# Optimization experiments

Measured on AMD Instinct MI355X. Metric: run time of the kernel, lower is better.

## Reference

```python
import jax, jax.numpy as jnp
import numpy as np

N_NODES = 50000
N_EDGES = 800000
D = 128


def setup_inputs() -> dict:
    key = jax.random.key(0)
    ks = jax.random.split(key, 7)
    return {
        "shape_features": jax.random.normal(ks[0], (N_NODES, D), dtype=jnp.float32),
        "W1": jax.random.normal(ks[1], (D, D), dtype=jnp.float32) * 0.05,
        "b1": jax.random.normal(ks[2], (D,), dtype=jnp.float32) * 0.05,
        "W2": jax.random.normal(ks[3], (D, D), dtype=jnp.float32) * 0.05,
        "b2": jax.random.normal(ks[4], (D,), dtype=jnp.float32) * 0.05,
        "edge_src": jax.random.randint(ks[5], (N_EDGES,), 0, N_NODES, dtype=jnp.int32),
        "edge_dst": jax.random.randint(ks[6], (N_EDGES,), 0, N_NODES, dtype=jnp.int32),
    }


def reference(shape_features, W1, b1, W2, b2, edge_src, edge_dst):
    # out1 = linear1(x)  (torch Linear: x @ W.T + b)
    out1 = jnp.einsum("nd,od->no", shape_features, W1) + b1
    # ragged neighbour gather + sum per destination node (segment reduce)
    aggr = jax.ops.segment_sum(shape_features[edge_src], edge_dst,
                               num_segments=shape_features.shape[0])
    # out = linear1(x) + linear2(aggr)
    return out1 + jnp.einsum("nd,od->no", aggr, W2) + b2
```

## Files before the change

### kernel.cpp

```cpp
#include <hip/hip_runtime.h>
#include <hip/hip_bf16.h>

#define DF 128
#define BSH 5
#define BNODES 32
#define NBMAX 2048
#define CHUNK 8192
#define BMAX 128
#define TILE 2048
#define ASTRIDE 68
#define SRCMASK 0x07ffffffu

typedef __attribute__((ext_vector_type(8))) short short8;
typedef __attribute__((ext_vector_type(4))) float floatx4;

__device__ __forceinline__ ushort f2bf(float f) {
    __hip_bfloat16 h = __float2bfloat16(f);
    return *reinterpret_cast<ushort*>(&h);
}

__global__ __launch_bounds__(256) void prep_kernel(
    const float* __restrict__ x, ushort* __restrict__ xbf, int n4,
    const float* __restrict__ W1, const float* __restrict__ W2,
    const float* __restrict__ b1, const float* __restrict__ b2,
    ushort* __restrict__ w1bf, ushort* __restrict__ w2bf, float* __restrict__ bias,
    const int* __restrict__ dst, int* __restrict__ histG,
    int n_edges, int B_, int nb)
{
    __shared__ int h[NBMAX];
    int bid = blockIdx.x;
    if (bid < B_) {
        for (int j = threadIdx.x; j < nb; j += 256) h[j] = 0;
        __syncthreads();
        int base = bid * CHUNK;
#pragma unroll 4
        for (int i = 0; i < CHUNK / 256; ++i) {
            int e = base + i * 256 + threadIdx.x;
            if (e < n_edges) atomicAdd(&h[dst[e] >> BSH], 1);
        }
        __syncthreads();
        for (int j = threadIdx.x; j < nb; j += 256)
            histG[bid * nb + j] = h[j];
    } else if (bid < B_ + 64) {
        int i = (bid - B_) * 256 + threadIdx.x;
        if (i < DF * DF) {
            w1bf[i] = f2bf(W1[i]);
            w2bf[i] = f2bf(W2[i]);
        }
        if (i < DF) bias[i] = b1[i] + b2[i];
    } else {
        int i = (bid - B_ - 64) * 256 + threadIdx.x;
        if (i < n4) {
            float4 v = reinterpret_cast<const float4*>(x)[i];
            ushort4 o;
            o.x = f2bf(v.x); o.y = f2bf(v.y); o.z = f2bf(v.z); o.w = f2bf(v.w);
            reinterpret_cast<ushort4*>(xbf)[i] = o;
        }
    }
}

__global__ __launch_bounds__(256) void scan_local_kernel(
    const int* __restrict__ cnt, int* __restrict__ offs,
    int* __restrict__ bsum, int n)
{
    __shared__ int sd[256];
    int t = threadIdx.x;
    int base = blockIdx.x * 1024 + t * 4;

    int4 v = make_int4(0, 0, 0, 0);
    if (base + 3 < n) {
        v = *reinterpret_cast<const int4*>(cnt + base);
    } else {
        if (base + 0 < n) v.x = cnt[base + 0];
        if (base + 1 < n) v.y = cnt[base + 1];
        if (base + 2 < n) v.z = cnt[base + 2];
        if (base + 3 < n) v.w = cnt[base + 3];
    }
    int s = v.x + v.y + v.z + v.w;
    sd[t] = s;
    __syncthreads();
    for (int off = 1; off < 256; off <<= 1) {
        int u = (t >= off) ? sd[t - off] : 0;
        __syncthreads();
        sd[t] += u;
        __syncthreads();
    }
    int incl = sd[t];
    int excl = incl - s;
    if (t == 255) bsum[blockIdx.x] = incl;

    int p0 = excl, p1 = p0 + v.x, p2 = p1 + v.y, p3 = p2 + v.z;
    if (base + 0 < n) offs[base + 0] = p0;
    if (base + 1 < n) offs[base + 1] = p1;
    if (base + 2 < n) offs[base + 2] = p2;
    if (base + 3 < n) offs[base + 3] = p3;
}

__global__ __launch_bounds__(1024) void scan_bsum_kernel(
    int* __restrict__ bsum, int nb2)
{
    __shared__ int sd[1024];
    int t = threadIdx.x;
    int v = (t < nb2) ? bsum[t] : 0;
    sd[t] = v;
    __syncthreads();
    for (int off = 1; off < 1024; off <<= 1) {
        int u = (t >= off) ? sd[t - off] : 0;
        __syncthreads();
        sd[t] += u;
        __syncthreads();
    }
    if (t < nb2) bsum[t] = sd[t] - v;
}

__global__ __launch_bounds__(1024) void bin_kernel(
    const int* __restrict__ src, const int* __restrict__ dst,
    const int* __restrict__ histS, const int* __restrict__ bsum,
    uint* __restrict__ pairs, int n_edges, int B_, int nb)
{
    __shared__ int  cur[NBMAX];
    __shared__ uint stage[CHUNK];
    int blk = blockIdx.x;
    for (int j = threadIdx.x; j < nb; j += 1024) {
        int idx = blk * nb + j;
        cur[j] = histS[idx] + bsum[idx >> 10];
    }
    __syncthreads();
    int base = blk * CHUNK;
    int cnt = n_edges - base; if (cnt > CHUNK) cnt = CHUNK;
    for (int i = threadIdx.x; i < cnt; i += 1024) {
        int e = base + i;
        int d = dst[e];
        int j = d >> BSH;
        int p = atomicAdd(&cur[j], 1);
        stage[p - base] = (uint)src[e] | ((uint)(d & (BNODES - 1)) << 27);
    }
    __syncthreads();
    for (int i = threadIdx.x; i < cnt; i += 1024)
        pairs[base + i] = stage[i];
}

__global__ __launch_bounds__(256) void agg_gemm_kernel(
    const ushort* __restrict__ xbf, const uint* __restrict__ pairs,
    const int* __restrict__ histS, const int* __restrict__ bsum,
    const ushort* __restrict__ w1, const ushort* __restrict__ w2,
    const float* __restrict__ bias, float* __restrict__ out,
    int n_nodes, int n_edges, int B_, int nb, int flat)
{
    __shared__ uint raw[TILE];
    __shared__ uint sorted[TILE];
    __shared__ uint abuf[BNODES * ASTRIDE];
    __shared__ int  rstart[BMAX];
    __shared__ int  rexcl[BMAX + 1];
    __shared__ int hcnt[BNODES];
    __shared__ int hoff[BNODES + 1];
    __shared__ int hcur[BNODES];

    int blk  = blockIdx.x;
    int node0 = blk * BNODES;
    int wave = threadIdx.x >> 6;
    int lane = threadIdx.x & 63;

    auto loadOffs = [&](int idx) -> int {
        if (idx >= flat) return n_edges;
        return histS[idx] + bsum[idx >> 10];
    };

    if (threadIdx.x < B_) {
        int idx = threadIdx.x * nb + blk;
        int s = loadOffs(idx);
        rstart[threadIdx.x] = s;
        rexcl[threadIdx.x]  = loadOffs(idx + 1) - s;
    }
    __syncthreads();
    if (threadIdx.x < 64) {
        int c0 = (lane < B_) ? rexcl[lane] : 0;
        int c1 = (64 + lane < B_) ? rexcl[64 + lane] : 0;
        int s0 = c0, s1 = c1;
#pragma unroll
        for (int off = 1; off < 64; off <<= 1) {
            int u0 = __shfl_up(s0, off);
            int u1 = __shfl_up(s1, off);
            if (lane >= off) { s0 += u0; s1 += u1; }
        }
        int t0 = __shfl(s0, 63);
        int t1 = __shfl(s1, 63);
        if (lane < B_) rexcl[lane] = s0 - c0;
        if (64 + lane < B_) rexcl[64 + lane] = t0 + s1 - c1;
        if (lane == 0) rexcl[B_] = t0 + t1;
    }
    __syncthreads();
    int total = rexcl[B_];

    const uint* xv = reinterpret_cast<const uint*>(xbf);
    float2 acc[8];
#pragma unroll
    for (int i = 0; i < 8; ++i) acc[i] = make_float2(0.f, 0.f);

    for (int t0 = 0; t0 < total; t0 += TILE) {
        int cnt = total - t0; if (cnt > TILE) cnt = TILE;

        if (threadIdx.x < BNODES) hcnt[threadIdx.x] = 0;
        __syncthreads();

        for (int i = threadIdx.x; i < cnt; i += 256) {
            int t = t0 + i;
            int lo = 0, hi = B_;
            while (lo + 1 < hi) {
                int mid = (lo + hi) >> 1;
                if (rexcl[mid] <= t) lo = mid; else hi = mid;
            }
            uint pk = pairs[rstart[lo] + (t - rexcl[lo])];
            raw[i] = pk;
            atomicAdd(&hcnt[pk >> 27], 1);
        }
        __syncthreads();

        if (threadIdx.x < 64) {
            int v = (lane < BNODES) ? hcnt[lane] : 0;
#pragma unroll
            for (int off = 1; off < BNODES; off <<= 1) {
                int u = __shfl_up(v, off);
                if (lane >= off) v += u;
            }
            if (lane < BNODES) {
                hoff[lane + 1] = v;
                hcur[lane] = v - hcnt[lane];
            }
            if (lane == 0) hoff[0] = 0;
        }
        __syncthreads();

        for (int i = threadIdx.x; i < cnt; i += 256) {
            uint pk = raw[i];
            int p = atomicAdd(&hcur[pk >> 27], 1);
            sorted[p] = pk & SRCMASK;
        }
        __syncthreads();

#pragma unroll
        for (int i = 0; i < 8; ++i) {
            int nl = wave * 8 + i;
            int j0 = hoff[nl], j1 = hoff[nl + 1];
            float2 a = acc[i];
            int j = j0;
            for (; j + 7 < j1; j += 8) {
                uint u0 = xv[(size_t)sorted[j + 0] * 64 + lane];
                uint u1 = xv[(size_t)sorted[j + 1] * 64 + lane];
                uint u2 = xv[(size_t)sorted[j + 2] * 64 + lane];
                uint u3 = xv[(size_t)sorted[j + 3] * 64 + lane];
                uint u4 = xv[(size_t)sorted[j + 4] * 64 + lane];
                uint u5 = xv[(size_t)sorted[j + 5] * 64 + lane];
                uint u6 = xv[(size_t)sorted[j + 6] * 64 + lane];
                uint u7 = xv[(size_t)sorted[j + 7] * 64 + lane];
                a.x += __uint_as_float(u0 << 16) + __uint_as_float(u1 << 16)
                     + __uint_as_float(u2 << 16) + __uint_as_float(u3 << 16)
                     + __uint_as_float(u4 << 16) + __uint_as_float(u5 << 16)
                     + __uint_as_float(u6 << 16) + __uint_as_float(u7 << 16);
                a.y += __uint_as_float(u0 & 0xffff0000u) + __uint_as_float(u1 & 0xffff0000u)
                     + __uint_as_float(u2 & 0xffff0000u) + __uint_as_float(u3 & 0xffff0000u)
                     + __uint_as_float(u4 & 0xffff0000u) + __uint_as_float(u5 & 0xffff0000u)
                     + __uint_as_float(u6 & 0xffff0000u) + __uint_as_float(u7 & 0xffff0000u);
            }
            for (; j + 3 < j1; j += 4) {
                uint u0 = xv[(size_t)sorted[j + 0] * 64 + lane];
                uint u1 = xv[(size_t)sorted[j + 1] * 64 + lane];
                uint u2 = xv[(size_t)sorted[j + 2] * 64 + lane];
                uint u3 = xv[(size_t)sorted[j + 3] * 64 + lane];
                a.x += __uint_as_float(u0 << 16) + __uint_as_float(u1 << 16)
                     + __uint_as_float(u2 << 16) + __uint_as_float(u3 << 16);
                a.y += __uint_as_float(u0 & 0xffff0000u) + __uint_as_float(u1 & 0xffff0000u)
                     + __uint_as_float(u2 & 0xffff0000u) + __uint_as_float(u3 & 0xffff0000u);
            }
            for (; j < j1; ++j) {
                uint u = xv[(size_t)sorted[j] * 64 + lane];
                a.x += __uint_as_float(u << 16);
                a.y += __uint_as_float(u & 0xffff0000u);
            }
            acc[i] = a;
        }
        __syncthreads();
    }

#pragma unroll
    for (int i = 0; i < 8; ++i) {
        int nl = wave * 8 + i;
        abuf[nl * ASTRIDE + lane] =
            (uint)f2bf(acc[i].x) | ((uint)f2bf(acc[i].y) << 16);
    }
    __syncthreads();

    int quad = lane >> 4;
    int m    = lane & 15;
    int rg   = wave >> 1;
    int half = wave & 1;
    int rowL = rg * 16 + m;
    int rowG = node0 + rowL;
    int rowC = (rowG < n_nodes) ? rowG : (n_nodes - 1);

    short8 xa[4], aa[4];
#pragma unroll
    for (int ks = 0; ks < 4; ++ks) {
        xa[ks] = *reinterpret_cast<const short8*>(xbf + (size_t)rowC * DF + ks * 32 + quad * 8);
        aa[ks] = *reinterpret_cast<const short8*>(&abuf[rowL * ASTRIDE + ks * 16 + quad * 4]);
    }

    int nbase = node0 + rg * 16;
#pragma unroll
    for (int oi = 0; oi < 4; ++oi) {
        int ot = half * 4 + oi;
        int o = ot * 16 + m;
        floatx4 c = {0.f, 0.f, 0.f, 0.f};
#pragma unroll
        for (int ks = 0; ks < 4; ++ks) {
            short8 bf1 = *reinterpret_cast<const short8*>(w1 + (size_t)o * DF + ks * 32 + quad * 8);
            short8 bf2 = *reinterpret_cast<const short8*>(w2 + (size_t)o * DF + ks * 32 + quad * 8);
            c = __builtin_amdgcn_mfma_f32_16x16x32_bf16(xa[ks], bf1, c, 0, 0, 0);
            c = __builtin_amdgcn_mfma_f32_16x16x32_bf16(aa[ks], bf2, c, 0, 0, 0);
        }
        float bv = bias[o];
#pragma unroll
        for (int r = 0; r < 4; ++r) {
            int row = nbase + quad * 4 + r;
            if (row < n_nodes) out[(size_t)row * DF + o] = c[r] + bv;
        }
    }
}

extern "C" void kernel_launch(void* const* d_in, const int* in_sizes, int n_in,
                              void* d_out, int out_size, void* d_ws, size_t ws_size,
                              hipStream_t stream) {
    const float* x  = (const float*)d_in[0];
    const float* W1 = (const float*)d_in[1];
    const float* b1 = (const float*)d_in[2];
    const float* W2 = (const float*)d_in[3];
    const float* b2 = (const float*)d_in[4];
    const int* esrc = (const int*)d_in[5];
    const int* edst = (const int*)d_in[6];
    float* out = (float*)d_out;

    int n_nodes = in_sizes[0] / DF;
    int n_edges = in_sizes[5];

    int nb = (n_nodes + BNODES - 1) >> BSH;
    int B_ = (n_edges + CHUNK - 1) / CHUNK;
    int flat = nb * B_;

    char* ws = (char*)d_ws;
    ushort* xbf   = (ushort*)ws;                 ws += (size_t)n_nodes * DF * 2;
    ushort* w1bf  = (ushort*)ws;                 ws += (size_t)DF * DF * 2;
    ushort* w2bf  = (ushort*)ws;                 ws += (size_t)DF * DF * 2;
    float*  bias  = (float*)ws;                  ws += (size_t)DF * 4;
    int*    histG = (int*)ws;                    ws += (size_t)flat * 4;
    int*    histS = (int*)ws;                    ws += (size_t)(flat + 1) * 4;
    int*    bsum  = (int*)ws;                    ws += 1024 * 4;
    uint*   pairs = (uint*)ws;

    int n4 = n_nodes * DF / 4;
    int prep_blocks = B_ + 64 + (n4 + 255) / 256;
    prep_kernel<<<prep_blocks, 256, 0, stream>>>(
        x, xbf, n4, W1, W2, b1, b2, w1bf, w2bf, bias,
        edst, histG, n_edges, B_, nb);

    int nb2 = (flat + 1023) / 1024;
    scan_local_kernel<<<nb2, 256, 0, stream>>>(histG, histS, bsum, flat);
    scan_bsum_kernel<<<1, 1024, 0, stream>>>(bsum, nb2);

    bin_kernel<<<B_, 1024, 0, stream>>>(esrc, edst, histS, bsum, pairs, n_edges, B_, nb);

    agg_gemm_kernel<<<nb, 256, 0, stream>>>(
        xbf, pairs, histS, bsum, w1bf, w2bf, bias, out,
        n_nodes, n_edges, B_, nb, flat);
}
```

Before: 178.0 us.

## Replace per-chunk histogram scans with global atomic histogram and last-block scan

```diff
diff --git a/kernel.cpp b/kernel.cpp
--- a/kernel.cpp
+++ b/kernel.cpp
@@ -5,8 +5,8 @@
 #define BSH 5
 #define BNODES 32
 #define NBMAX 2048
-#define CHUNK 8192
-#define BMAX 128
+#define PCHUNK 8192
+#define BCHUNK 4096
 #define TILE 2048
 #define ASTRIDE 68
 #define SRCMASK 0x07ffffffu
@@ -24,32 +24,69 @@
     const float* __restrict__ W1, const float* __restrict__ W2,
     const float* __restrict__ b1, const float* __restrict__ b2,
     ushort* __restrict__ w1bf, ushort* __restrict__ w2bf, float* __restrict__ bias,
-    const int* __restrict__ dst, int* __restrict__ histG,
-    int n_edges, int B_, int nb)
+    const int* __restrict__ dst, int* __restrict__ ghist, int* __restrict__ done,
+    int* __restrict__ gbase, int* __restrict__ gcur,
+    int n_edges, int PH, int nb)
 {
     __shared__ int h[NBMAX];
+    __shared__ int isLast;
     int bid = blockIdx.x;
-    if (bid < B_) {
+    if (bid < PH) {
         for (int j = threadIdx.x; j < nb; j += 256) h[j] = 0;
         __syncthreads();
-        int base = bid * CHUNK;
+        int base = bid * PCHUNK;
 #pragma unroll 4
-        for (int i = 0; i < CHUNK / 256; ++i) {
+        for (int i = 0; i < PCHUNK / 256; ++i) {
             int e = base + i * 256 + threadIdx.x;
             if (e < n_edges) atomicAdd(&h[dst[e] >> BSH], 1);
         }
         __syncthreads();
-        for (int j = threadIdx.x; j < nb; j += 256)
-            histG[bid * nb + j] = h[j];
-    } else if (bid < B_ + 64) {
-        int i = (bid - B_) * 256 + threadIdx.x;
+        for (int j = threadIdx.x; j < nb; j += 256) {
+            int c = h[j];
+            if (c) atomicAdd(&ghist[j], c);
+        }
+        __threadfence();
+        __syncthreads();
+        if (threadIdx.x == 0) isLast = (atomicAdd(done, 1) == PH - 1);
+        __syncthreads();
+        if (isLast) {
+            int b0 = threadIdx.x * 8;
+            int vals[8];
+            int s = 0;
+#pragma unroll
+            for (int k = 0; k < 8; ++k) {
+                int idx = b0 + k;
+                int v = (idx < nb)
+                    ? __hip_atomic_load(&ghist[idx], __ATOMIC_RELAXED,
+                                        __HIP_MEMORY_SCOPE_AGENT)
+                    : 0;
+                vals[k] = v; s += v;
+            }
+            h[threadIdx.x] = s;
+            __syncthreads();
+            for (int off = 1; off < 256; off <<= 1) {
+                int u = (threadIdx.x >= off) ? h[threadIdx.x - off] : 0;
+                __syncthreads();
+                h[threadIdx.x] += u;
+                __syncthreads();
+            }
+            int run = h[threadIdx.x] - s;
+#pragma unroll
+            for (int k = 0; k < 8; ++k) {
+                int idx = b0 + k;
+                if (idx < nb) { gbase[idx] = run; gcur[idx] = run; run += vals[k]; }
+            }
+            if (threadIdx.x == 0) gbase[nb] = n_edges;
+        }
+    } else if (bid < PH + 64) {
+        int i = (bid - PH) * 256 + threadIdx.x;
         if (i < DF * DF) {
             w1bf[i] = f2bf(W1[i]);
             w2bf[i] = f2bf(W2[i]);
         }
         if (i < DF) bias[i] = b1[i] + b2[i];
     } else {
-        int i = (bid - B_ - 64) * 256 + threadIdx.x;
+        int i = (bid - PH - 64) * 256 + threadIdx.x;
         if (i < n4) {
             float4 v = reinterpret_cast<const float4*>(x)[i];
             ushort4 o;
@@ -59,160 +96,81 @@
     }
 }
 
-__global__ __launch_bounds__(256) void scan_local_kernel(
-    const int* __restrict__ cnt, int* __restrict__ offs,
-    int* __restrict__ bsum, int n)
+__global__ __launch_bounds__(512) void bin_kernel(
+    const int* __restrict__ src, const int* __restrict__ dst,
+    int* __restrict__ gcur, uint* __restrict__ pairs, int n_edges, int nb)
 {
-    __shared__ int sd[256];
-    int t = threadIdx.x;
-    int base = blockIdx.x * 1024 + t * 4;
-
-    int4 v = make_int4(0, 0, 0, 0);
-    if (base + 3 < n) {
-        v = *reinterpret_cast<const int4*>(cnt + base);
-    } else {
-        if (base + 0 < n) v.x = cnt[base + 0];
-        if (base + 1 < n) v.y = cnt[base + 1];
-        if (base + 2 < n) v.z = cnt[base + 2];
-        if (base + 3 < n) v.w = cnt[base + 3];
-    }
-    int s = v.x + v.y + v.z + v.w;
-    sd[t] = s;
+    __shared__ int h[NBMAX];
+    int tid = threadIdx.x;
+    for (int j = tid; j < nb; j += 512) h[j] = 0;
     __syncthreads();
-    for (int off = 1; off < 256; off <<= 1) {
-        int u = (t >= off) ? sd[t - off] : 0;
-        __syncthreads();
-        sd[t] += u;
-        __syncthreads();
-    }
-    int incl = sd[t];
-    int excl = incl - s;
-    if (t == 255) bsum[blockIdx.x] = incl;
-
-    int p0 = excl, p1 = p0 + v.x, p2 = p1 + v.y, p3 = p2 + v.z;
-    if (base + 0 < n) offs[base + 0] = p0;
-    if (base + 1 < n) offs[base + 1] = p1;
-    if (base + 2 < n) offs[base + 2] = p2;
-    if (base + 3 < n) offs[base + 3] = p3;
-}
-
-__global__ __launch_bounds__(1024) void scan_bsum_kernel(
-    int* __restrict__ bsum, int nb2)
+    int base = blockIdx.x * BCHUNK;
+    int d[8], sv[8];
+#pragma unroll
+    for (int k = 0; k < 8; ++k) {
+        int i = base + k * 512 + tid;
+        bool ok = i < n_edges;
+        d[k]  = ok ? dst[i] : -1;
+        sv[k] = ok ? src[i] : 0;
+        if (ok) atomicAdd(&h[d[k] >> BSH], 1);
+    }
+    __syncthreads();
+    for (int j = tid; j < nb; j += 512) {
+        int c = h[j];
+        if (c) h[j] = atomicAdd(&gcur[j], c);
+    }
+    __syncthreads();
+#pragma unroll
+    for (int k = 0; k < 8; ++k) {
+        if (d[k] >= 0) {
+            int p = atomicAdd(&h[d[k] >> BSH], 1);
+            pairs[p] = (uint)sv[k] | ((uint)(d[k] & (BNODES - 1)) << 27);
+        }
+    }
+}
+
+__global__ __launch_bounds__(256, 6) void agg_gemm_kernel(
+    const ushort* __restrict__ xbf, const uint* __restrict__ pairs,
+    const int* __restrict__ gbase,
+    const ushort* __restrict__ w1, const ushort* __restrict__ w2,
+    const float* __restrict__ bias, float* __restrict__ out, int n_nodes)
 {
-    __shared__ int sd[1024];
-    int t = threadIdx.x;
-    int v = (t < nb2) ? bsum[t] : 0;
-    sd[t] = v;
-    __syncthreads();
-    for (int off = 1; off < 1024; off <<= 1) {
-        int u = (t >= off) ? sd[t - off] : 0;
-        __syncthreads();
-        sd[t] += u;
-        __syncthreads();
-    }
-    if (t < nb2) bsum[t] = sd[t] - v;
-}
-
-__global__ __launch_bounds__(1024) void bin_kernel(
-    const int* __restrict__ src, const int* __restrict__ dst,
-    const int* __restrict__ histS, const int* __restrict__ bsum,
-    uint* __restrict__ pairs, int n_edges, int B_, int nb)
-{
-    __shared__ int  cur[NBMAX];
-    __shared__ uint stage[CHUNK];
-    int blk = blockIdx.x;
-    for (int j = threadIdx.x; j < nb; j += 1024) {
-        int idx = blk * nb + j;
-        cur[j] = histS[idx] + bsum[idx >> 10];
-    }
-    __syncthreads();
-    int base = blk * CHUNK;
-    int cnt = n_edges - base; if (cnt > CHUNK) cnt = CHUNK;
-    for (int i = threadIdx.x; i < cnt; i += 1024) {
-        int e = base + i;
-        int d = dst[e];
-        int j = d >> BSH;
-        int p = atomicAdd(&cur[j], 1);
-        stage[p - base] = (uint)src[e] | ((uint)(d & (BNODES - 1)) << 27);
-    }
-    __syncthreads();
-    for (int i = threadIdx.x; i < cnt; i += 1024)
-        pairs[base + i] = stage[i];
-}
-
-__global__ __launch_bounds__(256) void agg_gemm_kernel(
-    const ushort* __restrict__ xbf, const uint* __restrict__ pairs,
-    const int* __restrict__ histS, const int* __restrict__ bsum,
-    const ushort* __restrict__ w1, const ushort* __restrict__ w2,
-    const float* __restrict__ bias, float* __restrict__ out,
-    int n_nodes, int n_edges, int B_, int nb, int flat)
-{
-    __shared__ uint raw[TILE];
     __shared__ uint sorted[TILE];
     __shared__ uint abuf[BNODES * ASTRIDE];
-    __shared__ int  rstart[BMAX];
-    __shared__ int  rexcl[BMAX + 1];
     __shared__ int hcnt[BNODES];
     __shared__ int hoff[BNODES + 1];
     __shared__ int hcur[BNODES];
 
-    int blk  = blockIdx.x;
+    int blk   = blockIdx.x;
     int node0 = blk * BNODES;
-    int wave = threadIdx.x >> 6;
-    int lane = threadIdx.x & 63;
-
-    auto loadOffs = [&](int idx) -> int {
-        if (idx >= flat) return n_edges;
-        return histS[idx] + bsum[idx >> 10];
-    };
-
-    if (threadIdx.x < B_) {
-        int idx = threadIdx.x * nb + blk;
-        int s = loadOffs(idx);
-        rstart[threadIdx.x] = s;
-        rexcl[threadIdx.x]  = loadOffs(idx + 1) - s;
-    }
-    __syncthreads();
-    if (threadIdx.x < 64) {
-        int c0 = (lane < B_) ? rexcl[lane] : 0;
-        int c1 = (64 + lane < B_) ? rexcl[64 + lane] : 0;
-        int s0 = c0, s1 = c1;
-#pragma unroll
-        for (int off = 1; off < 64; off <<= 1) {
-            int u0 = __shfl_up(s0, off);
-            int u1 = __shfl_up(s1, off);
-            if (lane >= off) { s0 += u0; s1 += u1; }
-        }
-        int t0 = __shfl(s0, 63);
-        int t1 = __shfl(s1, 63);
-        if (lane < B_) rexcl[lane] = s0 - c0;
-        if (64 + lane < B_) rexcl[64 + lane] = t0 + s1 - c1;
-        if (lane == 0) rexcl[B_] = t0 + t1;
-    }
-    __syncthreads();
-    int total = rexcl[B_];
-
-    const uint* xv = reinterpret_cast<const uint*>(xbf);
+    int wave  = threadIdx.x >> 6;
+    int lane  = threadIdx.x & 63;
+
+    int start = gbase[blk];
+    int end   = gbase[blk + 1];
+
+    const char* xu = (const char*)xbf;
+    uint lane4 = (uint)lane << 2;
+
     float2 acc[8];
 #pragma unroll
     for (int i = 0; i < 8; ++i) acc[i] = make_float2(0.f, 0.f);
 
-    for (int t0 = 0; t0 < total; t0 += TILE) {
-        int cnt = total - t0; if (cnt > TILE) cnt = TILE;
+    for (int t0 = start; t0 < end; t0 += TILE) {
+        int cnt = end - t0; if (cnt > TILE) cnt = TILE;
 
         if (threadIdx.x < BNODES) hcnt[threadIdx.x] = 0;
         __syncthreads();
 
-        for (int i = threadIdx.x; i < cnt; i += 256) {
-            int t = t0 + i;
-            int lo = 0, hi = B_;
-            while (lo + 1 < hi) {
-                int mid = (lo + hi) >> 1;
-                if (rexcl[mid] <= t) lo = mid; else hi = mid;
-            }
-            uint pk = pairs[rstart[lo] + (t - rexcl[lo])];
-            raw[i] = pk;
-            atomicAdd(&hcnt[pk >> 27], 1);
+        uint pk_[8];
+#pragma unroll
+        for (int k = 0; k < 8; ++k) {
+            int i = threadIdx.x + k * 256;
+            if (i < cnt) {
+                uint pk = pairs[t0 + i];
+                pk_[k] = pk;
+                atomicAdd(&hcnt[pk >> 27], 1);
+            }
         }
         __syncthreads();
 
@@ -231,10 +189,14 @@
         }
         __syncthreads();
 
-        for (int i = threadIdx.x; i < cnt; i += 256) {
-            uint pk = raw[i];
-            int p = atomicAdd(&hcur[pk >> 27], 1);
-            sorted[p] = pk & SRCMASK;
+#pragma unroll
+        for (int k = 0; k < 8; ++k) {
+            int i = threadIdx.x + k * 256;
+            if (i < cnt) {
+                uint pk = pk_[k];
+                int p = atomicAdd(&hcur[pk >> 27], 1);
+                sorted[p] = (pk & SRCMASK) << 8;
+            }
         }
         __syncthreads();
 
@@ -244,36 +206,29 @@
             int j0 = hoff[nl], j1 = hoff[nl + 1];
             float2 a = acc[i];
             int j = j0;
-            for (; j + 7 < j1; j += 8) {
-                uint u0 = xv[(size_t)sorted[j + 0] * 64 + lane];
-                uint u1 = xv[(size_t)sorted[j + 1] * 64 + lane];
-                uint u2 = xv[(size_t)sorted[j + 2] * 64 + lane];
-                uint u3 = xv[(size_t)sorted[j + 3] * 64 + lane];
-                uint u4 = xv[(size_t)sorted[j + 4] * 64 + lane];
-                uint u5 = xv[(size_t)sorted[j + 5] * 64 + lane];
-                uint u6 = xv[(size_t)sorted[j + 6] * 64 + lane];
-                uint u7 = xv[(size_t)sorted[j + 7] * 64 + lane];
-                a.x += __uint_as_float(u0 << 16) + __uint_as_float(u1 << 16)
-                     + __uint_as_float(u2 << 16) + __uint_as_float(u3 << 16)
-                     + __uint_as_float(u4 << 16) + __uint_as_float(u5 << 16)
-                     + __uint_as_float(u6 << 16) + __uint_as_float(u7 << 16);
-                a.y += __uint_as_float(u0 & 0xffff0000u) + __uint_as_float(u1 & 0xffff0000u)
-                     + __uint_as_float(u2 & 0xffff0000u) + __uint_as_float(u3 & 0xffff0000u)
-                     + __uint_as_float(u4 & 0xffff0000u) + __uint_as_float(u5 & 0xffff0000u)
-                     + __uint_as_float(u6 & 0xffff0000u) + __uint_as_float(u7 & 0xffff0000u);
+            for (; j + 15 < j1; j += 16) {
+                uint u[16];
+#pragma unroll
+                for (int k = 0; k < 16; ++k)
+                    u[k] = *(const uint*)(xu + (size_t)(sorted[j + k] + lane4));
+#pragma unroll
+                for (int k = 0; k < 16; ++k) {
+                    a.x += __uint_as_float(u[k] << 16);
+                    a.y += __uint_as_float(u[k] & 0xffff0000u);
+                }
             }
             for (; j + 3 < j1; j += 4) {
-                uint u0 = xv[(size_t)sorted[j + 0] * 64 + lane];
-                uint u1 = xv[(size_t)sorted[j + 1] * 64 + lane];
-                uint u2 = xv[(size_t)sorted[j + 2] * 64 + lane];
-                uint u3 = xv[(size_t)sorted[j + 3] * 64 + lane];
+                uint u0 = *(const uint*)(xu + (size_t)(sorted[j + 0] + lane4));
+                uint u1 = *(const uint*)(xu + (size_t)(sorted[j + 1] + lane4));
+                uint u2 = *(const uint*)(xu + (size_t)(sorted[j + 2] + lane4));
+                uint u3 = *(const uint*)(xu + (size_t)(sorted[j + 3] + lane4));
                 a.x += __uint_as_float(u0 << 16) + __uint_as_float(u1 << 16)
                      + __uint_as_float(u2 << 16) + __uint_as_float(u3 << 16);
                 a.y += __uint_as_float(u0 & 0xffff0000u) + __uint_as_float(u1 & 0xffff0000u)
                      + __uint_as_float(u2 & 0xffff0000u) + __uint_as_float(u3 & 0xffff0000u);
             }
             for (; j < j1; ++j) {
-                uint u = xv[(size_t)sorted[j] * 64 + lane];
+                uint u = *(const uint*)(xu + (size_t)(sorted[j] + lane4));
                 a.x += __uint_as_float(u << 16);
                 a.y += __uint_as_float(u & 0xffff0000u);
             }
@@ -343,32 +298,30 @@
     int n_edges = in_sizes[5];
 
     int nb = (n_nodes + BNODES - 1) >> BSH;
-    int B_ = (n_edges + CHUNK - 1) / CHUNK;
-    int flat = nb * B_;
+    int PH = (n_edges + PCHUNK - 1) / PCHUNK;
+    int BB = (n_edges + BCHUNK - 1) / BCHUNK;
 
     char* ws = (char*)d_ws;
     ushort* xbf   = (ushort*)ws;                 ws += (size_t)n_nodes * DF * 2;
     ushort* w1bf  = (ushort*)ws;                 ws += (size_t)DF * DF * 2;
     ushort* w2bf  = (ushort*)ws;                 ws += (size_t)DF * DF * 2;
     float*  bias  = (float*)ws;                  ws += (size_t)DF * 4;
-    int*    histG = (int*)ws;                    ws += (size_t)flat * 4;
-    int*    histS = (int*)ws;                    ws += (size_t)(flat + 1) * 4;
-    int*    bsum  = (int*)ws;                    ws += 1024 * 4;
+    int*    ghist = (int*)ws;                    ws += (size_t)(nb + 1) * 4;
+    int*    done  = ghist + nb;
+    int*    gbase = (int*)ws;                    ws += (size_t)(nb + 1) * 4;
+    int*    gcur  = (int*)ws;                    ws += (size_t)nb * 4;
     uint*   pairs = (uint*)ws;
 
+    hipMemsetAsync(ghist, 0, (size_t)(nb + 1) * sizeof(int), stream);
+
     int n4 = n_nodes * DF / 4;
-    int prep_blocks = B_ + 64 + (n4 + 255) / 256;
+    int prep_blocks = PH + 64 + (n4 + 255) / 256;
     prep_kernel<<<prep_blocks, 256, 0, stream>>>(
         x, xbf, n4, W1, W2, b1, b2, w1bf, w2bf, bias,
-        edst, histG, n_edges, B_, nb);
-
-    int nb2 = (flat + 1023) / 1024;
-    scan_local_kernel<<<nb2, 256, 0, stream>>>(histG, histS, bsum, flat);
-    scan_bsum_kernel<<<1, 1024, 0, stream>>>(bsum, nb2);
-
-    bin_kernel<<<B_, 1024, 0, stream>>>(esrc, edst, histS, bsum, pairs, n_edges, B_, nb);
+        edst, ghist, done, gbase, gcur, n_edges, PH, nb);
+
+    bin_kernel<<<BB, 512, 0, stream>>>(esrc, edst, gcur, pairs, n_edges, nb);
 
     agg_gemm_kernel<<<nb, 256, 0, stream>>>(
-        xbf, pairs, histS, bsum, w1bf, w2bf, bias, out,
-        n_nodes, n_edges, B_, nb, flat);
-}
+        xbf, pairs, gbase, w1bf, w2bf, bias, out, n_nodes);
+}
```

Result: slower. 188.1 us (+5.7%).

## Shrink node blocks to 16, fuse scan kernels, and widen gather unroll

Applied to the files above, without the earlier changes.

```diff
diff --git a/kernel.cpp b/kernel.cpp
--- a/kernel.cpp
+++ b/kernel.cpp
@@ -2,12 +2,12 @@
 #include <hip/hip_bf16.h>
 
 #define DF 128
-#define BSH 5
-#define BNODES 32
-#define NBMAX 2048
+#define BSH 4
+#define BNODES 16
+#define NBMAX 4096
 #define CHUNK 8192
 #define BMAX 128
-#define TILE 2048
+#define TILE 1024
 #define ASTRIDE 68
 #define SRCMASK 0x07ffffffu
 
@@ -24,7 +24,7 @@
     const float* __restrict__ W1, const float* __restrict__ W2,
     const float* __restrict__ b1, const float* __restrict__ b2,
     ushort* __restrict__ w1bf, ushort* __restrict__ w2bf, float* __restrict__ bias,
-    const int* __restrict__ dst, int* __restrict__ histG,
+    const int* __restrict__ dst, int* __restrict__ histG, int* __restrict__ sdone,
     int n_edges, int B_, int nb)
 {
     __shared__ int h[NBMAX];
@@ -48,6 +48,7 @@
             w2bf[i] = f2bf(W2[i]);
         }
         if (i < DF) bias[i] = b1[i] + b2[i];
+        if (bid == B_ && threadIdx.x == 0) *sdone = 0;
     } else {
         int i = (bid - B_ - 64) * 256 + threadIdx.x;
         if (i < n4) {
@@ -59,11 +60,12 @@
     }
 }
 
-__global__ __launch_bounds__(256) void scan_local_kernel(
+__global__ __launch_bounds__(256) void scan_kernel(
     const int* __restrict__ cnt, int* __restrict__ offs,
-    int* __restrict__ bsum, int n)
+    int* __restrict__ bsum, int* __restrict__ sdone, int n, int nb2)
 {
     __shared__ int sd[256];
+    __shared__ int isLast;
     int t = threadIdx.x;
     int base = blockIdx.x * 1024 + t * 4;
 
@@ -94,23 +96,40 @@
     if (base + 1 < n) offs[base + 1] = p1;
     if (base + 2 < n) offs[base + 2] = p2;
     if (base + 3 < n) offs[base + 3] = p3;
-}
-
-__global__ __launch_bounds__(1024) void scan_bsum_kernel(
-    int* __restrict__ bsum, int nb2)
-{
-    __shared__ int sd[1024];
-    int t = threadIdx.x;
-    int v = (t < nb2) ? bsum[t] : 0;
-    sd[t] = v;
-    __syncthreads();
-    for (int off = 1; off < 1024; off <<= 1) {
-        int u = (t >= off) ? sd[t - off] : 0;
-        __syncthreads();
-        sd[t] += u;
-        __syncthreads();
-    }
-    if (t < nb2) bsum[t] = sd[t] - v;
+
+    __threadfence();
+    __syncthreads();
+    if (t == 0) isLast = (atomicAdd(sdone, 1) == gridDim.x - 1);
+    __syncthreads();
+    if (isLast && t < 64) {
+        int b0 = t * 8;
+        int tv[8];
+        int run = 0;
+#pragma unroll
+        for (int k = 0; k < 8; ++k) {
+            int idx = b0 + k;
+            int u = (idx < nb2)
+                ? __hip_atomic_load(&bsum[idx], __ATOMIC_RELAXED,
+                                    __HIP_MEMORY_SCOPE_AGENT)
+                : 0;
+            tv[k] = u; run += u;
+        }
+        int laneTot = run;
+        int sI = laneTot;
+#pragma unroll
+        for (int off = 1; off < 64; off <<= 1) {
+            int u = __shfl_up(sI, off);
+            if (t >= off) sI += u;
+        }
+        int laneExcl = sI - laneTot;
+        int acc = laneExcl;
+#pragma unroll
+        for (int k = 0; k < 8; ++k) {
+            int idx = b0 + k;
+            if (idx < nb2) bsum[idx] = acc;
+            acc += tv[k];
+        }
+    }
 }
 
 __global__ __launch_bounds__(1024) void bin_kernel(
@@ -140,14 +159,13 @@
         pairs[base + i] = stage[i];
 }
 
-__global__ __launch_bounds__(256) void agg_gemm_kernel(
+__global__ __launch_bounds__(256, 6) void agg_gemm_kernel(
     const ushort* __restrict__ xbf, const uint* __restrict__ pairs,
     const int* __restrict__ histS, const int* __restrict__ bsum,
     const ushort* __restrict__ w1, const ushort* __restrict__ w2,
     const float* __restrict__ bias, float* __restrict__ out,
     int n_nodes, int n_edges, int B_, int nb, int flat)
 {
-    __shared__ uint raw[TILE];
     __shared__ uint sorted[TILE];
     __shared__ uint abuf[BNODES * ASTRIDE];
     __shared__ int  rstart[BMAX];
@@ -192,10 +210,12 @@
     __syncthreads();
     int total = rexcl[B_];
 
-    const uint* xv = reinterpret_cast<const uint*>(xbf);
-    float2 acc[8];
-#pragma unroll
-    for (int i = 0; i < 8; ++i) acc[i] = make_float2(0.f, 0.f);
+    const char* xu = (const char*)xbf;
+    uint lane4 = (uint)lane << 2;
+
+    float2 acc[4];
+#pragma unroll
+    for (int i = 0; i < 4; ++i) acc[i] = make_float2(0.f, 0.f);
 
     for (int t0 = 0; t0 < total; t0 += TILE) {
         int cnt = total - t0; if (cnt > TILE) cnt = TILE;
@@ -203,16 +223,21 @@
         if (threadIdx.x < BNODES) hcnt[threadIdx.x] = 0;
         __syncthreads();
 
-        for (int i = threadIdx.x; i < cnt; i += 256) {
-            int t = t0 + i;
-            int lo = 0, hi = B_;
-            while (lo + 1 < hi) {
-                int mid = (lo + hi) >> 1;
-                if (rexcl[mid] <= t) lo = mid; else hi = mid;
-            }
-            uint pk = pairs[rstart[lo] + (t - rexcl[lo])];
-            raw[i] = pk;
-            atomicAdd(&hcnt[pk >> 27], 1);
+        uint pk_[TILE / 256];
+#pragma unroll
+        for (int k = 0; k < TILE / 256; ++k) {
+            int i = threadIdx.x + k * 256;
+            if (i < cnt) {
+                int t = t0 + i;
+                int lo = 0, hi = B_;
+                while (lo + 1 < hi) {
+                    int mid = (lo + hi) >> 1;
+                    if (rexcl[mid] <= t) lo = mid; else hi = mid;
+                }
+                uint pk = pairs[rstart[lo] + (t - rexcl[lo])];
+                pk_[k] = pk;
+                atomicAdd(&hcnt[pk >> 27], 1);
+            }
         }
         __syncthreads();
 
@@ -231,49 +256,46 @@
         }
         __syncthreads();
 
-        for (int i = threadIdx.x; i < cnt; i += 256) {
-            uint pk = raw[i];
-            int p = atomicAdd(&hcur[pk >> 27], 1);
-            sorted[p] = pk & SRCMASK;
-        }
-        __syncthreads();
-
-#pragma unroll
-        for (int i = 0; i < 8; ++i) {
-            int nl = wave * 8 + i;
+#pragma unroll
+        for (int k = 0; k < TILE / 256; ++k) {
+            int i = threadIdx.x + k * 256;
+            if (i < cnt) {
+                uint pk = pk_[k];
+                int p = atomicAdd(&hcur[pk >> 27], 1);
+                sorted[p] = (pk & SRCMASK) << 8;
+            }
+        }
+        __syncthreads();
+
+#pragma unroll
+        for (int i = 0; i < 4; ++i) {
+            int nl = wave * 4 + i;
             int j0 = hoff[nl], j1 = hoff[nl + 1];
             float2 a = acc[i];
             int j = j0;
-            for (; j + 7 < j1; j += 8) {
-                uint u0 = xv[(size_t)sorted[j + 0] * 64 + lane];
-                uint u1 = xv[(size_t)sorted[j + 1] * 64 + lane];
-                uint u2 = xv[(size_t)sorted[j + 2] * 64 + lane];
-                uint u3 = xv[(size_t)sorted[j + 3] * 64 + lane];
-                uint u4 = xv[(size_t)sorted[j + 4] * 64 + lane];
-                uint u5 = xv[(size_t)sorted[j + 5] * 64 + lane];
-                uint u6 = xv[(size_t)sorted[j + 6] * 64 + lane];
-                uint u7 = xv[(size_t)sorted[j + 7] * 64 + lane];
-                a.x += __uint_as_float(u0 << 16) + __uint_as_float(u1 << 16)
-                     + __uint_as_float(u2 << 16) + __uint_as_float(u3 << 16)
-                     + __uint_as_float(u4 << 16) + __uint_as_float(u5 << 16)
-                     + __uint_as_float(u6 << 16) + __uint_as_float(u7 << 16);
-                a.y += __uint_as_float(u0 & 0xffff0000u) + __uint_as_float(u1 & 0xffff0000u)
-                     + __uint_as_float(u2 & 0xffff0000u) + __uint_as_float(u3 & 0xffff0000u)
-                     + __uint_as_float(u4 & 0xffff0000u) + __uint_as_float(u5 & 0xffff0000u)
-                     + __uint_as_float(u6 & 0xffff0000u) + __uint_as_float(u7 & 0xffff0000u);
+            for (; j + 15 < j1; j += 16) {
+                uint u[16];
+#pragma unroll
+                for (int k = 0; k < 16; ++k)
+                    u[k] = *(const uint*)(xu + (size_t)(sorted[j + k] + lane4));
+#pragma unroll
+                for (int k = 0; k < 16; ++k) {
+                    a.x += __uint_as_float(u[k] << 16);
+                    a.y += __uint_as_float(u[k] & 0xffff0000u);
+                }
             }
             for (; j + 3 < j1; j += 4) {
-                uint u0 = xv[(size_t)sorted[j + 0] * 64 + lane];
-                uint u1 = xv[(size_t)sorted[j + 1] * 64 + lane];
-                uint u2 = xv[(size_t)sorted[j + 2] * 64 + lane];
-                uint u3 = xv[(size_t)sorted[j + 3] * 64 + lane];
+                uint u0 = *(const uint*)(xu + (size_t)(sorted[j + 0] + lane4));
+                uint u1 = *(const uint*)(xu + (size_t)(sorted[j + 1] + lane4));
+                uint u2 = *(const uint*)(xu + (size_t)(sorted[j + 2] + lane4));
+                uint u3 = *(const uint*)(xu + (size_t)(sorted[j + 3] + lane4));
                 a.x += __uint_as_float(u0 << 16) + __uint_as_float(u1 << 16)
                      + __uint_as_float(u2 << 16) + __uint_as_float(u3 << 16);
                 a.y += __uint_as_float(u0 & 0xffff0000u) + __uint_as_float(u1 & 0xffff0000u)
                      + __uint_as_float(u2 & 0xffff0000u) + __uint_as_float(u3 & 0xffff0000u);
             }
             for (; j < j1; ++j) {
-                uint u = xv[(size_t)sorted[j] * 64 + lane];
+                uint u = *(const uint*)(xu + (size_t)(sorted[j] + lane4));
                 a.x += __uint_as_float(u << 16);
                 a.y += __uint_as_float(u & 0xffff0000u);
             }
@@ -283,8 +305,8 @@
     }
 
 #pragma unroll
-    for (int i = 0; i < 8; ++i) {
-        int nl = wave * 8 + i;
+    for (int i = 0; i < 4; ++i) {
+        int nl = wave * 4 + i;
         abuf[nl * ASTRIDE + lane] =
             (uint)f2bf(acc[i].x) | ((uint)f2bf(acc[i].y) << 16);
     }
@@ -292,23 +314,19 @@
 
     int quad = lane >> 4;
     int m    = lane & 15;
-    int rg   = wave >> 1;
-    int half = wave & 1;
-    int rowL = rg * 16 + m;
-    int rowG = node0 + rowL;
+    int rowG = node0 + m;
     int rowC = (rowG < n_nodes) ? rowG : (n_nodes - 1);
 
     short8 xa[4], aa[4];
 #pragma unroll
     for (int ks = 0; ks < 4; ++ks) {
         xa[ks] = *reinterpret_cast<const short8*>(xbf + (size_t)rowC * DF + ks * 32 + quad * 8);
-        aa[ks] = *reinterpret_cast<const short8*>(&abuf[rowL * ASTRIDE + ks * 16 + quad * 4]);
-    }
-
-    int nbase = node0 + rg * 16;
-#pragma unroll
-    for (int oi = 0; oi < 4; ++oi) {
-        int ot = half * 4 + oi;
+        aa[ks] = *reinterpret_cast<const short8*>(&abuf[m * ASTRIDE + ks * 16 + quad * 4]);
+    }
+
+#pragma unroll
+    for (int oi = 0; oi < 2; ++oi) {
+        int ot = wave * 2 + oi;
         int o = ot * 16 + m;
         floatx4 c = {0.f, 0.f, 0.f, 0.f};
 #pragma unroll
@@ -321,7 +339,7 @@
         float bv = bias[o];
 #pragma unroll
         for (int r = 0; r < 4; ++r) {
-            int row = nbase + quad * 4 + r;
+            int row = node0 + quad * 4 + r;
             if (row < n_nodes) out[(size_t)row * DF + o] = c[r] + bv;
         }
     }
@@ -353,18 +371,18 @@
     float*  bias  = (float*)ws;                  ws += (size_t)DF * 4;
     int*    histG = (int*)ws;                    ws += (size_t)flat * 4;
     int*    histS = (int*)ws;                    ws += (size_t)(flat + 1) * 4;
-    int*    bsum  = (int*)ws;                    ws += 1024 * 4;
+    int*    bsum  = (int*)ws;                    ws += 512 * 4;
+    int*    sdone = (int*)ws;                    ws += 4;
     uint*   pairs = (uint*)ws;
 
     int n4 = n_nodes * DF / 4;
     int prep_blocks = B_ + 64 + (n4 + 255) / 256;
     prep_kernel<<<prep_blocks, 256, 0, stream>>>(
         x, xbf, n4, W1, W2, b1, b2, w1bf, w2bf, bias,
-        edst, histG, n_edges, B_, nb);
+        edst, histG, sdone, n_edges, B_, nb);
 
     int nb2 = (flat + 1023) / 1024;
-    scan_local_kernel<<<nb2, 256, 0, stream>>>(histG, histS, bsum, flat);
-    scan_bsum_kernel<<<1, 1024, 0, stream>>>(bsum, nb2);
+    scan_kernel<<<nb2, 256, 0, stream>>>(histG, histS, bsum, sdone, flat, nb2);
 
     bin_kernel<<<B_, 1024, 0, stream>>>(esrc, edst, histS, bsum, pairs, n_edges, B_, nb);
 
```

After: 202.1 us. +13.6%, slower.
